# Performance work log

Hardware: AMD Instinct MI355X
Metric: run time of the kernel (lower is better)

Reference implementation:

```python
import jax, jax.numpy as jnp
import numpy as np

N_USERS, N_ITEMS, N_TAGS = 20000, 20000, 5000
N_NODES = N_USERS + N_ITEMS + N_TAGS  # 45000
EMB = 64
N_HOPS = 2
E_RAND = 600000
E = E_RAND + N_NODES  # 645000 edges incl. self-loops (add_residual)


def _xavier(k, shape):
    a = float(np.sqrt(6.0 / (shape[0] + shape[1])))
    return jax.random.uniform(k, shape, jnp.float32, -a, a)


def setup_inputs() -> dict:
    key = jax.random.key(0)
    ks = jax.random.split(key, 10)
    # COO graph indices; self-loops appended as in Recommender.add_residual
    head = jnp.concatenate([jax.random.randint(ks[0], (E_RAND,), 0, N_NODES),
                            jnp.arange(N_NODES)]).astype(jnp.int32)
    tail = jnp.concatenate([jax.random.randint(ks[1], (E_RAND,), 0, N_NODES),
                            jnp.arange(N_NODES)]).astype(jnp.int32)
    return {
        "user_emb": jax.random.normal(ks[2], (N_USERS, EMB), jnp.float32),
        "user_offset_emb": jax.random.normal(ks[3], (N_USERS, EMB), jnp.float32),
        "item_emb": jax.random.normal(ks[4], (N_ITEMS, EMB), jnp.float32),
        "item_offset_emb": jax.random.normal(ks[5], (N_ITEMS, EMB), jnp.float32),
        "tag_emb": jax.random.normal(ks[6], (N_TAGS, EMB), jnp.float32),
        "tag_offset": jax.random.normal(ks[7], (N_TAGS, EMB), jnp.float32),
        "W1": _xavier(ks[8], (EMB, EMB)),
        "b1": jnp.zeros((EMB,), jnp.float32),
        "W2": _xavier(ks[9], (EMB, EMB)),
        "b2": jnp.zeros((EMB,), jnp.float32),
        "head": head,
        "tail": tail,
    }


def _seg_softmax(src, idx, n_seg):
    # scatter_softmax: per-segment, per-feature softmax over edges
    m = jax.ops.segment_max(src, idx, num_segments=n_seg)
    m = jnp.where(jnp.isfinite(m), m, 0.0)
    e = jnp.exp(src - m[idx])
    s = jax.ops.segment_sum(e, idx, num_segments=n_seg)
    return e / s[idx]


def _center_net(embs, idx, n_seg, W1, b1, W2, b2):
    # CenterIntersection: Linear->relu->Linear->scatter_softmax->weighted scatter_sum
    h = jax.nn.relu(embs @ W1.T + b1)
    a = h @ W2.T + b2
    attn = _seg_softmax(a, idx, n_seg)
    return jax.ops.segment_sum(attn * embs, idx, num_segments=n_seg)


def _masked_seg_reduce(src, idx, mask, n_seg, union):
    # BoxOffsetIntersection over an edge subset: route masked-out edges to a
    # dummy segment; empty segments become 0 (torch_scatter semantics).
    idx2 = jnp.where(mask, idx, n_seg)
    if union:
        out = jax.ops.segment_max(src, idx2, num_segments=n_seg + 1)[:n_seg]
    else:
        out = jax.ops.segment_min(src, idx2, num_segments=n_seg + 1)[:n_seg]
    return jnp.where(jnp.isfinite(out), out, 0.0)


def reference(user_emb, user_offset_emb, item_emb, item_offset_emb, tag_emb,
              tag_offset, W1, b1, W2, b2, head, tail):
    nu, ni = N_USERS, N_ITEMS
    all_embs = jnp.concatenate([user_emb, item_emb, tag_emb], axis=0)
    all_off = jax.nn.relu(jnp.concatenate([user_offset_emb, item_offset_emb, tag_offset], axis=0))
    m_iu = (head < nu) & (tail >= nu) & (tail < nu + ni)   # user<-item edges
    m_ut = (head < nu) & (tail >= nu + ni)                 # user<-tag edges
    m_it = (head >= nu) & (head < nu + ni)                 # item head edges
    m_tg = head >= nu + ni                                 # tag head edges
    for _ in range(N_HOPS):
        emb_e = all_embs[tail]                       # [E, d] gather
        agg_emb = _center_net(emb_e, head, N_NODES, W1, b1, W2, b2)
        off_e = jax.nn.relu(all_off[tail])           # [E, d]
        iu = _masked_seg_reduce(off_e, head, m_iu, N_NODES, union=False)[:nu]
        ut = _masked_seg_reduce(off_e, head, m_ut, N_NODES, union=True)[:nu]
        # union of the two user offsets via scatter_min over user_union_idx + relu
        user_off = jax.nn.relu(jnp.minimum(iu, ut))
        item_off = _masked_seg_reduce(off_e, head, m_it, N_NODES, union=True)[nu:nu + ni]
        tag_off = _masked_seg_reduce(off_e, head, m_tg, N_NODES, union=False)[nu + ni:]
        # F.normalize (L2, dim=1)
        agg_emb = agg_emb / jnp.maximum(
            jnp.linalg.norm(agg_emb, axis=1, keepdims=True), 1e-12)
        all_embs = agg_emb
        all_off = jax.nn.relu(jnp.concatenate([user_off, item_off, tag_off], axis=0))
    return (all_embs[:nu], all_off[:nu],
            all_embs[nu:nu + ni], all_off[nu:nu + ni],
            all_embs[nu + ni:], all_off[nu + ni:])
```

## Files before the change

kernel.cpp:

```cpp
#include <hip/hip_runtime.h>
#include <math.h>

#define NU 20000
#define NI 20000
#define NT 5000
#define NN 45000
#define D  64
#define CAP 64
#define MBLK 704

typedef unsigned short u16;
typedef unsigned int u32;

typedef __attribute__((ext_vector_type(8))) short bf16x8;
typedef __attribute__((ext_vector_type(4))) float f32x4;

__device__ __forceinline__ float b2f(u16 u) {
  return __uint_as_float(((u32)u) << 16);
}
__device__ __forceinline__ u16 f2b(float f) {
  u32 x = __float_as_uint(f);
  u32 r = (x + 0x7fffu + ((x >> 16) & 1u)) >> 16;
  return (u16)r;
}
__device__ __forceinline__ const float* row3(int n, const float* a, const float* b, const float* c) {
  if (n < NU) return a + (size_t)n * D;
  if (n < NU + NI) return b + (size_t)(n - NU) * D;
  return c + (size_t)(n - NU - NI) * D;
}
__device__ __forceinline__ bf16x8 cvtf8(const float* p) {
  bf16x8 r;
#pragma unroll
  for (int j = 0; j < 8; ++j) r[j] = (short)f2b(p[j]);
  return r;
}

template <int FIRST>
__device__ __forceinline__ void mlp_body(
    int bid,
    const float* __restrict__ ue, const float* __restrict__ ie, const float* __restrict__ te,
    const float* __restrict__ uo, const float* __restrict__ io, const float* __restrict__ to,
    const u16* __restrict__ Xc, const u16* __restrict__ O2,
    const float* __restrict__ W1, const float* __restrict__ b1,
    const float* __restrict__ W2, const float* __restrict__ b2,
    uint2* __restrict__ PEO) {
  __shared__ u16 W1L[64][72];
  __shared__ u16 W2L[64][72];
  __shared__ u16 Hs[64][72];
  int tid = threadIdx.x;
  for (int i = tid; i < 4096; i += 256) {
    W1L[i >> 6][i & 63] = f2b(W1[i]);
    W2L[i >> 6][i & 63] = f2b(W2[i]);
  }
  __syncthreads();
  int w = tid >> 6, l = tid & 63;
  int lr = l & 15, kh = l >> 4;
  int nbase = bid * 64 + w * 16;
  int na = nbase + lr; if (na > NN - 1) na = NN - 1;
  bf16x8 A0, A1;
  if (FIRST) {
    const float* xr = row3(na, ue, ie, te);
    A0 = cvtf8(xr + kh * 8);
    A1 = cvtf8(xr + 32 + kh * 8);
  } else {
    A0 = *(const bf16x8*)(Xc + (size_t)na * 64 + kh * 8);
    A1 = *(const bf16x8*)(Xc + (size_t)na * 64 + 32 + kh * 8);
  }
#pragma unroll
  for (int ft = 0; ft < 4; ++ft) {
    int f = ft * 16 + lr;
    bf16x8 Bl = *(const bf16x8*)&W1L[f][kh * 8];
    bf16x8 Bh = *(const bf16x8*)&W1L[f][32 + kh * 8];
    f32x4 z = {0.f, 0.f, 0.f, 0.f};
    z = __builtin_amdgcn_mfma_f32_16x16x32_bf16(A0, Bl, z, 0, 0, 0);
    z = __builtin_amdgcn_mfma_f32_16x16x32_bf16(A1, Bh, z, 0, 0, 0);
    float bb = b1[f];
#pragma unroll
    for (int r = 0; r < 4; ++r)
      Hs[w * 16 + kh * 4 + r][f] = f2b(fmaxf(z[r] + bb, 0.f));
  }
  __syncthreads();
  bf16x8 A20 = *(const bf16x8*)&Hs[w * 16 + lr][kh * 8];
  bf16x8 A21 = *(const bf16x8*)&Hs[w * 16 + lr][32 + kh * 8];
#pragma unroll
  for (int ft = 0; ft < 4; ++ft) {
    int f = ft * 16 + lr;
    bf16x8 Bl = *(const bf16x8*)&W2L[f][kh * 8];
    bf16x8 Bh = *(const bf16x8*)&W2L[f][32 + kh * 8];
    f32x4 z = {0.f, 0.f, 0.f, 0.f};
    z = __builtin_amdgcn_mfma_f32_16x16x32_bf16(A20, Bl, z, 0, 0, 0);
    z = __builtin_amdgcn_mfma_f32_16x16x32_bf16(A21, Bh, z, 0, 0, 0);
    float bb = b2[f];
#pragma unroll
    for (int r = 0; r < 4; ++r) {
      int node = nbase + kh * 4 + r;
      if (node < NN) {
        float a = z[r] + bb;
        float p = __expf(fminf(fmaxf(a, -60.f), 60.f));
        u32 eo;
        if (FIRST) {
          float ev = row3(node, ue, ie, te)[f];
          float ov = fmaxf(row3(node, uo, io, to)[f], 0.f);
          eo = (u32)f2b(ev) | ((u32)f2b(ov) << 16);
        } else {
          u32 idx = ((u32)node << 6) + f;
          eo = (u32)Xc[idx] | ((u32)O2[idx] << 16);
        }
        uint2 v; v.x = __float_as_uint(p); v.y = eo;
        PEO[((size_t)node << 6) + f] = v;
      }
    }
  }
}

__global__ __launch_bounds__(256) void fused1_kernel(
    const float* __restrict__ ue, const float* __restrict__ ie, const float* __restrict__ te,
    const float* __restrict__ uo, const float* __restrict__ io, const float* __restrict__ to,
    const float* __restrict__ W1, const float* __restrict__ b1,
    const float* __restrict__ W2, const float* __restrict__ b2,
    const int* __restrict__ head, const int* __restrict__ tail, int E,
    uint2* __restrict__ PEO, int* __restrict__ cnt, u16* __restrict__ csr) {
  int bid = blockIdx.x;
  if (bid >= MBLK) {
    int i = (bid - MBLK) * 256 + threadIdx.x;
    if (i < E) {
      int h = head[i];
      int s = atomicAdd(&cnt[h], 1);
      if (s < CAP) __builtin_nontemporal_store((u16)tail[i], &csr[h * CAP + s]);
    }
    return;
  }
  mlp_body<1>(bid, ue, ie, te, uo, io, to, nullptr, nullptr, W1, b1, W2, b2, PEO);
}

__global__ __launch_bounds__(256) void mlp2_kernel(
    const u16* __restrict__ Xc, const u16* __restrict__ O2,
    const float* __restrict__ W1, const float* __restrict__ b1,
    const float* __restrict__ W2, const float* __restrict__ b2,
    uint2* __restrict__ PEO) {
  mlp_body<0>(blockIdx.x, nullptr, nullptr, nullptr, nullptr, nullptr, nullptr,
              Xc, O2, W1, b1, W2, b2, PEO);
}

template <int FINAL>
__global__ __launch_bounds__(256) void agg_kernel(
    const int* __restrict__ cnt, const u16* __restrict__ csr,
    const uint2* __restrict__ PEO,
    u16* __restrict__ Xco, u16* __restrict__ Oo, float* __restrict__ out) {
  int n = (blockIdx.x * blockDim.x + threadIdx.x) >> 6;
  int lane = threadIdx.x & 63;
  if (n >= NN) return;
  int cn = min(cnt[n], CAP);
  int tl = (lane < cn) ? (int)csr[n * CAP + lane] : 0;
  const char* Pb = (const char*)PEO;
  size_t lo = (size_t)(lane << 3);
  float ss0 = 0.f, ss1 = 0.f, ss2 = 0.f, ss3 = 0.f;
  float ts0 = 0.f, ts1 = 0.f, ts2 = 0.f, ts3 = 0.f;
  float mn0 = 3.4e38f, mn1 = 3.4e38f;
  float mx0 = -3.4e38f, mx1 = -3.4e38f;

#define LD(T) (*(const uint2*)(Pb + ((size_t)(u32)(T) << 9) + lo))
#define ACC(V, SS, TS)                                  \
  { float p_ = __uint_as_float((V).x);                  \
    float e_ = b2f((u16)((V).y & 0xffffu));             \
    SS += p_; TS = fmaf(p_, e_, TS); }
#define OV(V) b2f((u16)((V).y >> 16))

  if (n < NU) {
    int j = 0;
    for (; j + 7 < cn; j += 8) {
      int t0 = __shfl(tl, j),     t1 = __shfl(tl, j + 1);
      int t2 = __shfl(tl, j + 2), t3 = __shfl(tl, j + 3);
      int t4 = __shfl(tl, j + 4), t5 = __shfl(tl, j + 5);
      int t6 = __shfl(tl, j + 6), t7 = __shfl(tl, j + 7);
      uint2 v0 = LD(t0), v1 = LD(t1), v2 = LD(t2), v3 = LD(t3);
      uint2 v4 = LD(t4), v5 = LD(t5), v6 = LD(t6), v7 = LD(t7);
      ACC(v0, ss0, ts0) ACC(v1, ss1, ts1) ACC(v2, ss2, ts2) ACC(v3, ss3, ts3)
      ACC(v4, ss0, ts0) ACC(v5, ss1, ts1) ACC(v6, ss2, ts2) ACC(v7, ss3, ts3)
      if (t0 >= NU + NI) mx0 = fmaxf(mx0, OV(v0)); else if (t0 >= NU) mn0 = fminf(mn0, OV(v0));
      if (t1 >= NU + NI) mx1 = fmaxf(mx1, OV(v1)); else if (t1 >= NU) mn1 = fminf(mn1, OV(v1));
      if (t2 >= NU + NI) mx0 = fmaxf(mx0, OV(v2)); else if (t2 >= NU) mn0 = fminf(mn0, OV(v2));
      if (t3 >= NU + NI) mx1 = fmaxf(mx1, OV(v3)); else if (t3 >= NU) mn1 = fminf(mn1, OV(v3));
      if (t4 >= NU + NI) mx0 = fmaxf(mx0, OV(v4)); else if (t4 >= NU) mn0 = fminf(mn0, OV(v4));
      if (t5 >= NU + NI) mx1 = fmaxf(mx1, OV(v5)); else if (t5 >= NU) mn1 = fminf(mn1, OV(v5));
      if (t6 >= NU + NI) mx0 = fmaxf(mx0, OV(v6)); else if (t6 >= NU) mn0 = fminf(mn0, OV(v6));
      if (t7 >= NU + NI) mx1 = fmaxf(mx1, OV(v7)); else if (t7 >= NU) mn1 = fminf(mn1, OV(v7));
    }
    for (; j < cn; ++j) {
      int t = __shfl(tl, j);
      uint2 v = LD(t);
      ACC(v, ss0, ts0)
      if (t >= NU + NI) mx0 = fmaxf(mx0, OV(v)); else if (t >= NU) mn0 = fminf(mn0, OV(v));
    }
  } else if (n < NU + NI) {
    int j = 0;
    for (; j + 7 < cn; j += 8) {
      int t0 = __shfl(tl, j),     t1 = __shfl(tl, j + 1);
      int t2 = __shfl(tl, j + 2), t3 = __shfl(tl, j + 3);
      int t4 = __shfl(tl, j + 4), t5 = __shfl(tl, j + 5);
      int t6 = __shfl(tl, j + 6), t7 = __shfl(tl, j + 7);
      uint2 v0 = LD(t0), v1 = LD(t1), v2 = LD(t2), v3 = LD(t3);
      uint2 v4 = LD(t4), v5 = LD(t5), v6 = LD(t6), v7 = LD(t7);
      ACC(v0, ss0, ts0) ACC(v1, ss1, ts1) ACC(v2, ss2, ts2) ACC(v3, ss3, ts3)
      ACC(v4, ss0, ts0) ACC(v5, ss1, ts1) ACC(v6, ss2, ts2) ACC(v7, ss3, ts3)
      mx0 = fmaxf(mx0, OV(v0)); mx1 = fmaxf(mx1, OV(v1));
      mx0 = fmaxf(mx0, OV(v2)); mx1 = fmaxf(mx1, OV(v3));
      mx0 = fmaxf(mx0, OV(v4)); mx1 = fmaxf(mx1, OV(v5));
      mx0 = fmaxf(mx0, OV(v6)); mx1 = fmaxf(mx1, OV(v7));
    }
    for (; j < cn; ++j) {
      int t = __shfl(tl, j);
      uint2 v = LD(t);
      ACC(v, ss0, ts0)
      mx0 = fmaxf(mx0, OV(v));
    }
  } else {
    int j = 0;
    for (; j + 7 < cn; j += 8) {
      int t0 = __shfl(tl, j),     t1 = __shfl(tl, j + 1);
      int t2 = __shfl(tl, j + 2), t3 = __shfl(tl, j + 3);
      int t4 = __shfl(tl, j + 4), t5 = __shfl(tl, j + 5);
      int t6 = __shfl(tl, j + 6), t7 = __shfl(tl, j + 7);
      uint2 v0 = LD(t0), v1 = LD(t1), v2 = LD(t2), v3 = LD(t3);
      uint2 v4 = LD(t4), v5 = LD(t5), v6 = LD(t6), v7 = LD(t7);
      ACC(v0, ss0, ts0) ACC(v1, ss1, ts1) ACC(v2, ss2, ts2) ACC(v3, ss3, ts3)
      ACC(v4, ss0, ts0) ACC(v5, ss1, ts1) ACC(v6, ss2, ts2) ACC(v7, ss3, ts3)
      mn0 = fminf(mn0, OV(v0)); mn1 = fminf(mn1, OV(v1));
      mn0 = fminf(mn0, OV(v2)); mn1 = fminf(mn1, OV(v3));
      mn0 = fminf(mn0, OV(v4)); mn1 = fminf(mn1, OV(v5));
      mn0 = fminf(mn0, OV(v6)); mn1 = fminf(mn1, OV(v7));
    }
    for (; j < cn; ++j) {
      int t = __shfl(tl, j);
      uint2 v = LD(t);
      ACC(v, ss0, ts0)
      mn0 = fminf(mn0, OV(v));
    }
  }
#undef LD
#undef ACC
#undef OV

  float ssum = (ss0 + ss1) + (ss2 + ss3);
  float tsum = (ts0 + ts1) + (ts2 + ts3);
  float omin = fminf(mn0, mn1), omax = fmaxf(mx0, mx1);
  float agg = tsum / ssum;
  float sq = agg * agg;
#pragma unroll
  for (int msk = 1; msk < 64; msk <<= 1) sq += __shfl_xor(sq, msk);
  float outv = agg / fmaxf(sqrtf(sq), 1e-12f);
  float offv;
  if (n < NU) {
    float iu = (omin > 1e37f) ? 0.f : omin;
    float ut = (omax < -1e37f) ? 0.f : omax;
    offv = fmaxf(fminf(iu, ut), 0.f);
  } else if (n < NU + NI) {
    offv = fmaxf((omax < -1e37f) ? 0.f : omax, 0.f);
  } else {
    offv = fmaxf((omin > 1e37f) ? 0.f : omin, 0.f);
  }
  if (FINAL) {
    float* oe; float* oo;
    if (n < NU)           { oe = out + (size_t)n * D;
                            oo = out + (size_t)NU * D + (size_t)n * D; }
    else if (n < NU + NI) { int q = n - NU;
                            oe = out + (size_t)2 * NU * D + (size_t)q * D;
                            oo = oe + (size_t)NI * D; }
    else                  { int q = n - NU - NI;
                            oe = out + (size_t)(2 * NU + 2 * NI) * D + (size_t)q * D;
                            oo = oe + (size_t)NT * D; }
    __builtin_nontemporal_store(outv, &oe[lane]);
    __builtin_nontemporal_store(offv, &oo[lane]);
  } else {
    u32 idx = ((u32)n << 6) + lane;
    Xco[idx] = f2b(outv);
    Oo[idx] = f2b(offv);
  }
}

extern "C" void kernel_launch(void* const* d_in, const int* in_sizes, int n_in,
                              void* d_out, int out_size, void* d_ws, size_t ws_size,
                              hipStream_t stream) {
  const float* ue = (const float*)d_in[0];
  const float* uo = (const float*)d_in[1];
  const float* ie = (const float*)d_in[2];
  const float* io = (const float*)d_in[3];
  const float* te = (const float*)d_in[4];
  const float* to = (const float*)d_in[5];
  const float* W1 = (const float*)d_in[6];
  const float* b1 = (const float*)d_in[7];
  const float* W2 = (const float*)d_in[8];
  const float* b2 = (const float*)d_in[9];
  const int* head = (const int*)d_in[10];
  const int* tail = (const int*)d_in[11];
  int E = in_sizes[10];

  const size_t NE = (size_t)NN * 64;
  uint2* PEO = (uint2*)d_ws;
  u16* Xc  = (u16*)(PEO + NE);
  u16* O2  = Xc + NE;
  int* cnt = (int*)(O2 + NE);
  u16* csr = (u16*)(cnt + NN);

  hipMemsetAsync(cnt, 0, NN * sizeof(int), stream);
  int sb = (E + 255) / 256;

  fused1_kernel<<<MBLK + sb, 256, 0, stream>>>(
      ue, ie, te, uo, io, to, W1, b1, W2, b2, head, tail, E, PEO, cnt, csr);
  int ab = (NN + 3) / 4;
  agg_kernel<0><<<ab, 256, 0, stream>>>(cnt, csr, PEO, Xc, O2, nullptr);

  mlp2_kernel<<<MBLK, 256, 0, stream>>>(Xc, O2, W1, b1, W2, b2, PEO);
  agg_kernel<1><<<ab, 256, 0, stream>>>(cnt, csr, PEO, nullptr, nullptr, (float*)d_out);
}
```

Measured before the change: 154.8 us.

## Compact gathered payload to bf16, split offsets, tile CSR per 32 nodes, specialize agg

The softmax weight becomes bf16 and is packed with the embedding into one u32, and the offset goes to its own bf16 array. The gather payload per edge drops from 8 bytes to 4+2. The CSR is stored in a 32-node interleaved tile layout that one block loads into shared memory with a single vector load, and the aggregation kernel is split into three launches specialized by node type. This removes per-node branching and warp shuffles, but adds extra launches, a second gather stream per edge, and bf16 rounding of the softmax weights, which reduces accuracy.

Measured after the change: 234.5 us. 51.5% more time.

```diff
diff --git a/kernel.cpp b/kernel.cpp
--- a/kernel.cpp
+++ b/kernel.cpp
@@ -8,6 +8,7 @@
 #define D  64
 #define CAP 64
 #define MBLK 704
+#define NG 1407
 
 typedef unsigned short u16;
 typedef unsigned int u32;
@@ -40,10 +41,10 @@
     int bid,
     const float* __restrict__ ue, const float* __restrict__ ie, const float* __restrict__ te,
     const float* __restrict__ uo, const float* __restrict__ io, const float* __restrict__ to,
-    const u16* __restrict__ Xc, const u16* __restrict__ O2,
+    const u16* __restrict__ Xc,
     const float* __restrict__ W1, const float* __restrict__ b1,
     const float* __restrict__ W2, const float* __restrict__ b2,
-    uint2* __restrict__ PEO) {
+    u32* __restrict__ PE, u16* __restrict__ O1) {
   __shared__ u16 W1L[64][72];
   __shared__ u16 W2L[64][72];
   __shared__ u16 Hs[64][72];
@@ -97,17 +98,15 @@
       if (node < NN) {
         float a = z[r] + bb;
         float p = __expf(fminf(fmaxf(a, -60.f), 60.f));
-        u32 eo;
+        u32 idx = ((u32)node << 6) + f;
+        u32 eb;
         if (FIRST) {
-          float ev = row3(node, ue, ie, te)[f];
-          float ov = fmaxf(row3(node, uo, io, to)[f], 0.f);
-          eo = (u32)f2b(ev) | ((u32)f2b(ov) << 16);
+          eb = f2b(row3(node, ue, ie, te)[f]);
+          O1[idx] = f2b(fmaxf(row3(node, uo, io, to)[f], 0.f));
         } else {
-          u32 idx = ((u32)node << 6) + f;
-          eo = (u32)Xc[idx] | ((u32)O2[idx] << 16);
+          eb = Xc[idx];
         }
-        uint2 v; v.x = __float_as_uint(p); v.y = eo;
-        PEO[((size_t)node << 6) + f] = v;
+        PE[idx] = (u32)f2b(p) | (eb << 16);
       }
     }
   }
@@ -119,163 +118,156 @@
     const float* __restrict__ W1, const float* __restrict__ b1,
     const float* __restrict__ W2, const float* __restrict__ b2,
     const int* __restrict__ head, const int* __restrict__ tail, int E,
-    uint2* __restrict__ PEO, int* __restrict__ cnt, u16* __restrict__ csr) {
+    u32* __restrict__ PE, u16* __restrict__ O1,
+    int* __restrict__ cnt, u16* __restrict__ csr) {
   int bid = blockIdx.x;
   if (bid >= MBLK) {
     int i = (bid - MBLK) * 256 + threadIdx.x;
     if (i < E) {
       int h = head[i];
       int s = atomicAdd(&cnt[h], 1);
-      if (s < CAP) __builtin_nontemporal_store((u16)tail[i], &csr[h * CAP + s]);
+      if (s < CAP) csr[((h >> 5) << 11) + (s << 5) + (h & 31)] = (u16)tail[i];
     }
     return;
   }
-  mlp_body<1>(bid, ue, ie, te, uo, io, to, nullptr, nullptr, W1, b1, W2, b2, PEO);
+  mlp_body<1>(bid, ue, ie, te, uo, io, to, nullptr, W1, b1, W2, b2, PE, O1);
 }
 
 __global__ __launch_bounds__(256) void mlp2_kernel(
-    const u16* __restrict__ Xc, const u16* __restrict__ O2,
+    const u16* __restrict__ Xc,
     const float* __restrict__ W1, const float* __restrict__ b1,
     const float* __restrict__ W2, const float* __restrict__ b2,
-    uint2* __restrict__ PEO) {
+    u32* __restrict__ PE) {
   mlp_body<0>(blockIdx.x, nullptr, nullptr, nullptr, nullptr, nullptr, nullptr,
-              Xc, O2, W1, b1, W2, b2, PEO);
-}
-
-template <int FINAL>
+              Xc, W1, b1, W2, b2, PE, nullptr);
+}
+
+template <int FINAL, int TYPE>
 __global__ __launch_bounds__(256) void agg_kernel(
     const int* __restrict__ cnt, const u16* __restrict__ csr,
-    const uint2* __restrict__ PEO,
-    u16* __restrict__ Xco, u16* __restrict__ Oo, float* __restrict__ out) {
-  int n = (blockIdx.x * blockDim.x + threadIdx.x) >> 6;
-  int lane = threadIdx.x & 63;
-  if (n >= NN) return;
-  int cn = min(cnt[n], CAP);
-  int tl = (lane < cn) ? (int)csr[n * CAP + lane] : 0;
-  const char* Pb = (const char*)PEO;
-  size_t lo = (size_t)(lane << 3);
-  float ss0 = 0.f, ss1 = 0.f, ss2 = 0.f, ss3 = 0.f;
-  float ts0 = 0.f, ts1 = 0.f, ts2 = 0.f, ts3 = 0.f;
-  float mn0 = 3.4e38f, mn1 = 3.4e38f;
-  float mx0 = -3.4e38f, mx1 = -3.4e38f;
-
-#define LD(T) (*(const uint2*)(Pb + ((size_t)(u32)(T) << 9) + lo))
+    const u32* __restrict__ PE, const u16* __restrict__ O,
+    u16* __restrict__ Xco, u16* __restrict__ Oo, float* __restrict__ out, int g0) {
+  __shared__ u16 s_csr[CAP * 32];
+  __shared__ int s_cnt[32];
+  int g = g0 + blockIdx.x;
+  int tid = threadIdx.x;
+  {
+    const uint4* src = (const uint4*)(csr + ((size_t)g << 11));
+    ((uint4*)s_csr)[tid] = src[tid];
+    if (tid < 32) s_cnt[tid] = cnt[(g << 5) + tid];
+  }
+  __syncthreads();
+  int w = tid >> 6, lane = tid & 63;
+  for (int nl = w; nl < 32; nl += 4) {
+    int n = (g << 5) + nl;
+    if (n >= NN) break;
+    int cn = min(s_cnt[nl], CAP);
+    float ss0 = 0.f, ss1 = 0.f, ss2 = 0.f, ss3 = 0.f;
+    float ts0 = 0.f, ts1 = 0.f, ts2 = 0.f, ts3 = 0.f;
+    float mn0 = 3.4e38f, mn1 = 3.4e38f;
+    float mx0 = -3.4e38f, mx1 = -3.4e38f;
+
 #define ACC(V, SS, TS)                                  \
-  { float p_ = __uint_as_float((V).x);                  \
-    float e_ = b2f((u16)((V).y & 0xffffu));             \
-    SS += p_; TS = fmaf(p_, e_, TS); }
-#define OV(V) b2f((u16)((V).y >> 16))
-
-  if (n < NU) {
+    { float p_ = b2f((u16)((V) & 0xffffu));             \
+      float e_ = b2f((u16)((V) >> 16));                 \
+      SS += p_; TS = fmaf(p_, e_, TS); }
+
     int j = 0;
     for (; j + 7 < cn; j += 8) {
-      int t0 = __shfl(tl, j),     t1 = __shfl(tl, j + 1);
-      int t2 = __shfl(tl, j + 2), t3 = __shfl(tl, j + 3);
-      int t4 = __shfl(tl, j + 4), t5 = __shfl(tl, j + 5);
-      int t6 = __shfl(tl, j + 6), t7 = __shfl(tl, j + 7);
-      uint2 v0 = LD(t0), v1 = LD(t1), v2 = LD(t2), v3 = LD(t3);
-      uint2 v4 = LD(t4), v5 = LD(t5), v6 = LD(t6), v7 = LD(t7);
+      int t0 = s_csr[((j + 0) << 5) + nl], t1 = s_csr[((j + 1) << 5) + nl];
+      int t2 = s_csr[((j + 2) << 5) + nl], t3 = s_csr[((j + 3) << 5) + nl];
+      int t4 = s_csr[((j + 4) << 5) + nl], t5 = s_csr[((j + 5) << 5) + nl];
+      int t6 = s_csr[((j + 6) << 5) + nl], t7 = s_csr[((j + 7) << 5) + nl];
+      u32 v0 = PE[((u32)t0 << 6) + lane], v1 = PE[((u32)t1 << 6) + lane];
+      u32 v2 = PE[((u32)t2 << 6) + lane], v3 = PE[((u32)t3 << 6) + lane];
+      u32 v4 = PE[((u32)t4 << 6) + lane], v5 = PE[((u32)t5 << 6) + lane];
+      u32 v6 = PE[((u32)t6 << 6) + lane], v7 = PE[((u32)t7 << 6) + lane];
+      float o0 = b2f(O[((u32)t0 << 6) + lane]), o1 = b2f(O[((u32)t1 << 6) + lane]);
+      float o2 = b2f(O[((u32)t2 << 6) + lane]), o3 = b2f(O[((u32)t3 << 6) + lane]);
+      float o4 = b2f(O[((u32)t4 << 6) + lane]), o5 = b2f(O[((u32)t5 << 6) + lane]);
+      float o6 = b2f(O[((u32)t6 << 6) + lane]), o7 = b2f(O[((u32)t7 << 6) + lane]);
       ACC(v0, ss0, ts0) ACC(v1, ss1, ts1) ACC(v2, ss2, ts2) ACC(v3, ss3, ts3)
       ACC(v4, ss0, ts0) ACC(v5, ss1, ts1) ACC(v6, ss2, ts2) ACC(v7, ss3, ts3)
-      if (t0 >= NU + NI) mx0 = fmaxf(mx0, OV(v0)); else if (t0 >= NU) mn0 = fminf(mn0, OV(v0));
-      if (t1 >= NU + NI) mx1 = fmaxf(mx1, OV(v1)); else if (t1 >= NU) mn1 = fminf(mn1, OV(v1));
-      if (t2 >= NU + NI) mx0 = fmaxf(mx0, OV(v2)); else if (t2 >= NU) mn0 = fminf(mn0, OV(v2));
-      if (t3 >= NU + NI) mx1 = fmaxf(mx1, OV(v3)); else if (t3 >= NU) mn1 = fminf(mn1, OV(v3));
-      if (t4 >= NU + NI) mx0 = fmaxf(mx0, OV(v4)); else if (t4 >= NU) mn0 = fminf(mn0, OV(v4));
-      if (t5 >= NU + NI) mx1 = fmaxf(mx1, OV(v5)); else if (t5 >= NU) mn1 = fminf(mn1, OV(v5));
-      if (t6 >= NU + NI) mx0 = fmaxf(mx0, OV(v6)); else if (t6 >= NU) mn0 = fminf(mn0, OV(v6));
-      if (t7 >= NU + NI) mx1 = fmaxf(mx1, OV(v7)); else if (t7 >= NU) mn1 = fminf(mn1, OV(v7));
+      if (TYPE == 0) {
+        if (t0 >= NU + NI) mx0 = fmaxf(mx0, o0); else if (t0 >= NU) mn0 = fminf(mn0, o0);
+        if (t1 >= NU + NI) mx1 = fmaxf(mx1, o1); else if (t1 >= NU) mn1 = fminf(mn1, o1);
+        if (t2 >= NU + NI) mx0 = fmaxf(mx0, o2); else if (t2 >= NU) mn0 = fminf(mn0, o2);
+        if (t3 >= NU + NI) mx1 = fmaxf(mx1, o3); else if (t3 >= NU) mn1 = fminf(mn1, o3);
+        if (t4 >= NU + NI) mx0 = fmaxf(mx0, o4); else if (t4 >= NU) mn0 = fminf(mn0, o4);
+        if (t5 >= NU + NI) mx1 = fmaxf(mx1, o5); else if (t5 >= NU) mn1 = fminf(mn1, o5);
+        if (t6 >= NU + NI) mx0 = fmaxf(mx0, o6); else if (t6 >= NU) mn0 = fminf(mn0, o6);
+        if (t7 >= NU + NI) mx1 = fmaxf(mx1, o7); else if (t7 >= NU) mn1 = fminf(mn1, o7);
+      } else if (TYPE == 1) {
+        mx0 = fmaxf(mx0, o0); mx1 = fmaxf(mx1, o1);
+        mx0 = fmaxf(mx0, o2); mx1 = fmaxf(mx1, o3);
+        mx0 = fmaxf(mx0, o4); mx1 = fmaxf(mx1, o5);
+        mx0 = fmaxf(mx0, o6); mx1 = fmaxf(mx1, o7);
+      } else {
+        mn0 = fminf(mn0, o0); mn1 = fminf(mn1, o1);
+        mn0 = fminf(mn0, o2); mn1 = fminf(mn1, o3);
+        mn0 = fminf(mn0, o4); mn1 = fminf(mn1, o5);
+        mn0 = fminf(mn0, o6); mn1 = fminf(mn1, o7);
+      }
     }
     for (; j < cn; ++j) {
-      int t = __shfl(tl, j);
-      uint2 v = LD(t);
+      int t = s_csr[(j << 5) + nl];
+      u32 v = PE[((u32)t << 6) + lane];
+      float o = b2f(O[((u32)t << 6) + lane]);
       ACC(v, ss0, ts0)
-      if (t >= NU + NI) mx0 = fmaxf(mx0, OV(v)); else if (t >= NU) mn0 = fminf(mn0, OV(v));
-    }
-  } else if (n < NU + NI) {
-    int j = 0;
-    for (; j + 7 < cn; j += 8) {
-      int t0 = __shfl(tl, j),     t1 = __shfl(tl, j + 1);
-      int t2 = __shfl(tl, j + 2), t3 = __shfl(tl, j + 3);
-      int t4 = __shfl(tl, j + 4), t5 = __shfl(tl, j + 5);
-      int t6 = __shfl(tl, j + 6), t7 = __shfl(tl, j + 7);
-      uint2 v0 = LD(t0), v1 = LD(t1), v2 = LD(t2), v3 = LD(t3);
-      uint2 v4 = LD(t4), v5 = LD(t5), v6 = LD(t6), v7 = LD(t7);
-      ACC(v0, ss0, ts0) ACC(v1, ss1, ts1) ACC(v2, ss2, ts2) ACC(v3, ss3, ts3)
-      ACC(v4, ss0, ts0) ACC(v5, ss1, ts1) ACC(v6, ss2, ts2) ACC(v7, ss3, ts3)
-      mx0 = fmaxf(mx0, OV(v0)); mx1 = fmaxf(mx1, OV(v1));
-      mx0 = fmaxf(mx0, OV(v2)); mx1 = fmaxf(mx1, OV(v3));
-      mx0 = fmaxf(mx0, OV(v4)); mx1 = fmaxf(mx1, OV(v5));
-      mx0 = fmaxf(mx0, OV(v6)); mx1 = fmaxf(mx1, OV(v7));
-    }
-    for (; j < cn; ++j) {
-      int t = __shfl(tl, j);
-      uint2 v = LD(t);
-      ACC(v, ss0, ts0)
-      mx0 = fmaxf(mx0, OV(v));
-    }
-  } else {
-    int j = 0;
-    for (; j + 7 < cn; j += 8) {
-      int t0 = __shfl(tl, j),     t1 = __shfl(tl, j + 1);
-      int t2 = __shfl(tl, j + 2), t3 = __shfl(tl, j + 3);
-      int t4 = __shfl(tl, j + 4), t5 = __shfl(tl, j + 5);
-      int t6 = __shfl(tl, j + 6), t7 = __shfl(tl, j + 7);
-      uint2 v0 = LD(t0), v1 = LD(t1), v2 = LD(t2), v3 = LD(t3);
-      uint2 v4 = LD(t4), v5 = LD(t5), v6 = LD(t6), v7 = LD(t7);
-      ACC(v0, ss0, ts0) ACC(v1, ss1, ts1) ACC(v2, ss2, ts2) ACC(v3, ss3, ts3)
-      ACC(v4, ss0, ts0) ACC(v5, ss1, ts1) ACC(v6, ss2, ts2) ACC(v7, ss3, ts3)
-      mn0 = fminf(mn0, OV(v0)); mn1 = fminf(mn1, OV(v1));
-      mn0 = fminf(mn0, OV(v2)); mn1 = fminf(mn1, OV(v3));
-      mn0 = fminf(mn0, OV(v4)); mn1 = fminf(mn1, OV(v5));
-      mn0 = fminf(mn0, OV(v6)); mn1 = fminf(mn1, OV(v7));
-    }
-    for (; j < cn; ++j) {
-      int t = __shfl(tl, j);
-      uint2 v = LD(t);
-      ACC(v, ss0, ts0)
-      mn0 = fminf(mn0, OV(v));
-    }
-  }
-#undef LD
+      if (TYPE == 0) {
+        if (t >= NU + NI) mx0 = fmaxf(mx0, o); else if (t >= NU) mn0 = fminf(mn0, o);
+      } else if (TYPE == 1) {
+        mx0 = fmaxf(mx0, o);
+      } else {
+        mn0 = fminf(mn0, o);
+      }
+    }
 #undef ACC
-#undef OV
-
-  float ssum = (ss0 + ss1) + (ss2 + ss3);
-  float tsum = (ts0 + ts1) + (ts2 + ts3);
-  float omin = fminf(mn0, mn1), omax = fmaxf(mx0, mx1);
-  float agg = tsum / ssum;
-  float sq = agg * agg;
-#pragma unroll
-  for (int msk = 1; msk < 64; msk <<= 1) sq += __shfl_xor(sq, msk);
-  float outv = agg / fmaxf(sqrtf(sq), 1e-12f);
-  float offv;
-  if (n < NU) {
-    float iu = (omin > 1e37f) ? 0.f : omin;
-    float ut = (omax < -1e37f) ? 0.f : omax;
-    offv = fmaxf(fminf(iu, ut), 0.f);
-  } else if (n < NU + NI) {
-    offv = fmaxf((omax < -1e37f) ? 0.f : omax, 0.f);
-  } else {
-    offv = fmaxf((omin > 1e37f) ? 0.f : omin, 0.f);
-  }
-  if (FINAL) {
-    float* oe; float* oo;
-    if (n < NU)           { oe = out + (size_t)n * D;
+
+    float ssum = (ss0 + ss1) + (ss2 + ss3);
+    float tsum = (ts0 + ts1) + (ts2 + ts3);
+    float omin = fminf(mn0, mn1), omax = fmaxf(mx0, mx1);
+    float agg = tsum / ssum;
+    float sq = agg * agg;
+#pragma unroll
+    for (int msk = 1; msk < 64; msk <<= 1) sq += __shfl_xor(sq, msk);
+    float outv = agg / fmaxf(sqrtf(sq), 1e-12f);
+    float offv;
+    if (TYPE == 0) {
+      float iu = (omin > 1e37f) ? 0.f : omin;
+      float ut = (omax < -1e37f) ? 0.f : omax;
+      offv = fmaxf(fminf(iu, ut), 0.f);
+    } else if (TYPE == 1) {
+      offv = fmaxf((omax < -1e37f) ? 0.f : omax, 0.f);
+    } else {
+      offv = fmaxf((omin > 1e37f) ? 0.f : omin, 0.f);
+    }
+    if (FINAL) {
+      float* oe; float* oo;
+      if (TYPE == 0)      { oe = out + (size_t)n * D;
                             oo = out + (size_t)NU * D + (size_t)n * D; }
-    else if (n < NU + NI) { int q = n - NU;
+      else if (TYPE == 1) { int q = n - NU;
                             oe = out + (size_t)2 * NU * D + (size_t)q * D;
                             oo = oe + (size_t)NI * D; }
-    else                  { int q = n - NU - NI;
+      else                { int q = n - NU - NI;
                             oe = out + (size_t)(2 * NU + 2 * NI) * D + (size_t)q * D;
                             oo = oe + (size_t)NT * D; }
-    __builtin_nontemporal_store(outv, &oe[lane]);
-    __builtin_nontemporal_store(offv, &oo[lane]);
-  } else {
-    u32 idx = ((u32)n << 6) + lane;
-    Xco[idx] = f2b(outv);
-    Oo[idx] = f2b(offv);
-  }
+      __builtin_nontemporal_store(outv, &oe[lane]);
+      __builtin_nontemporal_store(offv, &oo[lane]);
+    } else {
+      u32 idx = ((u32)n << 6) + lane;
+      Xco[idx] = f2b(outv);
+      Oo[idx] = f2b(offv);
+    }
+  }
+}
+
+template <int FINAL>
+static void launch_agg(const int* cnt, const u16* csr, const u32* PE, const u16* O,
+                       u16* Xco, u16* Oo, float* out, hipStream_t stream) {
+  agg_kernel<FINAL, 0><<<625, 256, 0, stream>>>(cnt, csr, PE, O, Xco, Oo, out, 0);
+  agg_kernel<FINAL, 1><<<625, 256, 0, stream>>>(cnt, csr, PE, O, Xco, Oo, out, 625);
+  agg_kernel<FINAL, 2><<<157, 256, 0, stream>>>(cnt, csr, PE, O, Xco, Oo, out, 1250);
 }
 
 extern "C" void kernel_launch(void* const* d_in, const int* in_sizes, int n_in,
@@ -296,20 +288,20 @@
   int E = in_sizes[10];
 
   const size_t NE = (size_t)NN * 64;
-  uint2* PEO = (uint2*)d_ws;
-  u16* Xc  = (u16*)(PEO + NE);
-  u16* O2  = Xc + NE;
-  int* cnt = (int*)(O2 + NE);
+  u32* PE  = (u32*)d_ws;
+  u16* O1  = (u16*)(PE + NE);
+  u16* O2  = O1 + NE;
+  u16* Xc  = O2 + NE;
+  int* cnt = (int*)(Xc + NE);
   u16* csr = (u16*)(cnt + NN);
 
   hipMemsetAsync(cnt, 0, NN * sizeof(int), stream);
-  int sb = (E + 255) / 256;
-
-  fused1_kernel<<<MBLK + sb, 256, 0, stream>>>(
-      ue, ie, te, uo, io, to, W1, b1, W2, b2, head, tail, E, PEO, cnt, csr);
-  int ab = (NN + 3) / 4;
-  agg_kernel<0><<<ab, 256, 0, stream>>>(cnt, csr, PEO, Xc, O2, nullptr);
-
-  mlp2_kernel<<<MBLK, 256, 0, stream>>>(Xc, O2, W1, b1, W2, b2, PEO);
-  agg_kernel<1><<<ab, 256, 0, stream>>>(cnt, csr, PEO, nullptr, nullptr, (float*)d_out);
-}
+  int nsb = (E + 255) / 256;
+
+  fused1_kernel<<<MBLK + nsb, 256, 0, stream>>>(
+      ue, ie, te, uo, io, to, W1, b1, W2, b2, head, tail, E, PE, O1, cnt, csr);
+  launch_agg<0>(cnt, csr, PE, O1, Xc, O2, nullptr, stream);
+
+  mlp2_kernel<<<MBLK, 256, 0, stream>>>(Xc, W1, b1, W2, b2, PE);
+  launch_agg<1>(cnt, csr, PE, O2, nullptr, nullptr, (float*)d_out, stream);
+}
```
